# Kernel optimization log

Measured on AMD Instinct MI355X. Metric: run time of the kernel, lower is better.

## Reference

```python
import jax, jax.numpy as jnp
import numpy as np

B, T, C, H, D = 4, 2048, 1024, 16, 64
EPS = 1e-5

def setup_inputs() -> dict:
    key = jax.random.key(0)
    ks = jax.random.split(key, 8)
    s = lambda fan_in: 1.0 / np.sqrt(fan_in)
    return {
        'x': jax.random.normal(ks[0], (B, T, C), jnp.float32),
        'wq': jax.random.normal(ks[1], (H, C, D), jnp.float32) * s(C),
        'wk': jax.random.normal(ks[2], (H, C, D), jnp.float32) * s(C),
        'wv': jax.random.normal(ks[3], (H, C, D), jnp.float32) * s(C),
        'w_proj': jax.random.normal(ks[4], (C, C), jnp.float32) * s(C),
        'b_proj': jnp.zeros((C,), jnp.float32),
        'w1': jax.random.normal(ks[5], (C, 4 * C), jnp.float32) * s(C),
        'b1': jnp.zeros((4 * C,), jnp.float32),
        'w2': jax.random.normal(ks[6], (4 * C, C), jnp.float32) * s(4 * C),
        'b2': jnp.zeros((C,), jnp.float32),
        'g1': jnp.ones((C,), jnp.float32),
        'be1': jnp.zeros((C,), jnp.float32),
        'g2': jnp.ones((C,), jnp.float32),
        'be2': jnp.zeros((C,), jnp.float32),
    }

def layer_norm(x, g, b):
    mu = jnp.mean(x, axis=-1, keepdims=True)
    var = jnp.mean(jnp.square(x - mu), axis=-1, keepdims=True)
    return (x - mu) * jax.lax.rsqrt(var + EPS) * g + b

def reference(x, wq, wk, wv, w_proj, b_proj, w1, b1, w2, b2, g1, be1, g2, be2):
    # --- attention (pre-LN) ---
    xn = layer_norm(x, g1, be1)
    q = jnp.einsum('btc,hcd->bhtd', xn, wq)
    k = jnp.einsum('btc,hcd->bhtd', xn, wk)
    v = jnp.einsum('btc,hcd->bhtd', xn, wv)
    # NOTE: original scales by full embedding dim C (not head size)
    scores = jnp.einsum('bhtd,bhsd->bhts', q, k) * (C ** -0.5)
    causal = jnp.tril(jnp.ones((T, T), bool))
    scores = jnp.where(causal, scores, -jnp.inf)
    wei = jax.nn.softmax(scores, axis=-1)
    attn = jnp.einsum('bhts,bhsd->bhtd', wei, v)
    attn = attn.transpose(0, 2, 1, 3).reshape(B, T, C)  # concat heads
    x = x + attn @ w_proj + b_proj
    # --- FFN (pre-LN) ---
    xn2 = layer_norm(x, g2, be2)
    h = jax.nn.relu(xn2 @ w1 + b1)
    x = x + h @ w2 + b2
    return x
```

## Files before the change

kernel.cpp:

```cpp
#include <hip/hip_runtime.h>
#include <hip/hip_bf16.h>

#define B_ 4
#define T_ 2048
#define C_ 1024
#define H_ 16
#define D_ 64
#define M_ (B_*T_)

typedef unsigned short ushort;
typedef __attribute__((ext_vector_type(8))) short short8;
typedef __attribute__((ext_vector_type(8))) unsigned short ushort8;
typedef __attribute__((ext_vector_type(4))) float floatx4;
typedef __attribute__((ext_vector_type(4))) unsigned int uintx4;

static __device__ __forceinline__ float bf2f(ushort u) {
    unsigned int x = ((unsigned int)u) << 16;
    return __builtin_bit_cast(float, x);
}
static __device__ __forceinline__ ushort f2bf(float f) {
    unsigned int x = __builtin_bit_cast(unsigned int, f);
    unsigned int r = (x + 0x7fffu + ((x >> 16) & 1u)) >> 16;
    return (ushort)r;
}

typedef const __attribute__((address_space(1))) unsigned int gu32;
typedef __attribute__((address_space(3))) unsigned int lu32;
static __device__ __forceinline__ void glds16(const void* g, void* l) {
    __builtin_amdgcn_global_load_lds((gu32*)g, (lu32*)l, 16, 0, 0);
}

__global__ __launch_bounds__(256) void ln_kernel(
    const float* __restrict__ x, const float* __restrict__ g,
    const float* __restrict__ be, ushort* __restrict__ out)
{
    int row = blockIdx.x;
    int tid = threadIdx.x;
    const float* xr = x + (size_t)row * C_;
    float v[4];
    float s = 0.f, s2 = 0.f;
#pragma unroll
    for (int i = 0; i < 4; i++) {
        float t = xr[tid + i * 256];
        v[i] = t; s += t; s2 += t * t;
    }
#pragma unroll
    for (int off = 32; off; off >>= 1) {
        s  += __shfl_down(s, off);
        s2 += __shfl_down(s2, off);
    }
    __shared__ float rs[4], rs2[4];
    __shared__ float smu, srstd;
    int w = tid >> 6;
    if ((tid & 63) == 0) { rs[w] = s; rs2[w] = s2; }
    __syncthreads();
    if (tid == 0) {
        float ts  = rs[0] + rs[1] + rs[2] + rs[3];
        float ts2 = rs2[0] + rs2[1] + rs2[2] + rs2[3];
        float mu  = ts * (1.f / C_);
        float var = ts2 * (1.f / C_) - mu * mu;
        smu = mu; srstd = rsqrtf(var + 1e-5f);
    }
    __syncthreads();
    float mu = smu, r = srstd;
#pragma unroll
    for (int i = 0; i < 4; i++) {
        int c = tid + i * 256;
        out[(size_t)row * C_ + c] = f2bf((v[i] - mu) * r * g[c] + be[c]);
    }
}

__global__ __launch_bounds__(256) void transpose_conv(
    const float* __restrict__ in, ushort* __restrict__ out,
    int R, int Cn, long long in_bstride, long long out_bstride)
{
    __shared__ float tile[32][33];
    const float* ip = in + (size_t)blockIdx.z * in_bstride;
    ushort* op = out + (size_t)blockIdx.z * out_bstride;
    int tx = threadIdx.x;
    int ty = threadIdx.y;
    int c0 = blockIdx.x * 32, r0 = blockIdx.y * 32;
#pragma unroll
    for (int i = 0; i < 32; i += 8) {
        tile[ty + i][tx] = ip[(size_t)(r0 + ty + i) * Cn + c0 + tx];
    }
    __syncthreads();
#pragma unroll
    for (int i = 0; i < 32; i += 8) {
        int oc = c0 + ty + i;
        int orr = r0 + tx;
        op[(size_t)oc * R + orr] = f2bf(tile[tx][ty + i]);
    }
}

__global__ __launch_bounds__(256) void vtrans_kernel(
    const ushort* __restrict__ qkv, ushort* __restrict__ VtG)
{
    int bh = blockIdx.y;
    int b = bh >> 4, h = bh & 15;
    int j0 = blockIdx.x * 64;
    int tid = threadIdx.x;
    __shared__ unsigned int X[64 * 33];
    const ushort* Vg = qkv + (size_t)(b * T_) * 3072 + 2048 + h * 64;
#pragma unroll
    for (int it = 0; it < 2; it++) {
        int j = (tid >> 3) + it * 32;
        int dp = (tid & 7) * 4;
        uintx4 val = *(const uintx4*)(Vg + (size_t)(j0 + j) * 3072 + dp * 2);
#pragma unroll
        for (int k = 0; k < 4; k++) X[j * 33 + dp + k] = val[k];
    }
    __syncthreads();
    int dp = tid >> 3, jc = tid & 7;
    unsigned int v[8];
#pragma unroll
    for (int jj = 0; jj < 8; jj++) v[jj] = X[(jc * 8 + jj) * 33 + dp];
    ushort8 lo, hi;
#pragma unroll
    for (int jj = 0; jj < 8; jj++) {
        lo[jj] = (ushort)(v[jj] & 0xffffu);
        hi[jj] = (ushort)(v[jj] >> 16);
    }
    size_t r0 = ((size_t)(h * 256 + 4 * (2 * dp) + b)) * T_ + j0 + jc * 8;
    size_t r1 = ((size_t)(h * 256 + 4 * (2 * dp + 1) + b)) * T_ + j0 + jc * 8;
    *(ushort8*)&VtG[r0] = lo;
    *(ushort8*)&VtG[r1] = hi;
}

template<bool OUTBF16, bool BIAS, bool RELU, bool RESID>
__global__ __launch_bounds__(512, 2) void gemm3b_kernel(
    const ushort* __restrict__ A,
    const ushort* __restrict__ Bt,
    const float* __restrict__ bias,
    const float* __restrict__ resid,
    void* __restrict__ Cout,
    int Mdim, int Ndim, int K)
{
    __shared__ ushort As[3][256 * 64];
    __shared__ ushort Bs[3][128 * 64];

    int gridX = gridDim.x;
    int nwg = gridX * gridDim.y;
    int bid = blockIdx.y * gridX + blockIdx.x;
    int cpx = nwg >> 3;
    int swz = (bid & 7) * cpx + (bid >> 3);
    int bx = swz % gridX, by = swz / gridX;
    int m0 = by * 256, n0 = bx * 128;

    int tid = threadIdx.x;
    int wave = tid >> 6, lane = tid & 63;
    int quad = lane >> 4, l16 = lane & 15;
    int wr = wave >> 1, wc = wave & 1;
    int wm = wr * 64, wn = wc * 64;
    int lrow = lane >> 3;
    int lchunk = (lane & 7) ^ (lrow & 7);

    floatx4 acc[4][4] = {};
    int nt = K >> 6;

    auto stage = [&](int t, int sb) {
        int k0 = t << 6;
#pragma unroll
        for (int it = 0; it < 4; it++) {
            int rb = it * 64 + wave * 8;
            glds16(A + (size_t)(m0 + rb + lrow) * K + k0 + lchunk * 8, &As[sb][rb * 64]);
        }
#pragma unroll
        for (int it = 0; it < 2; it++) {
            int rb = it * 64 + wave * 8;
            glds16(Bt + (size_t)(n0 + rb + lrow) * K + k0 + lchunk * 8, &Bs[sb][rb * 64]);
        }
    };

    stage(0, 0);
    stage(1, 1);
    asm volatile("s_waitcnt vmcnt(6)" ::: "memory");
    __builtin_amdgcn_s_barrier();
    asm volatile("" ::: "memory");

    int s0 = 0, s1 = 1, s2 = 2;
    for (int t = 0; t < nt; ++t) {
        short8 af[4][2], bfv[4][2];
#pragma unroll
        for (int kk = 0; kk < 2; kk++) {
            int c = kk * 4 + quad;
#pragma unroll
            for (int mi = 0; mi < 4; mi++) {
                int r = wm + mi * 16 + l16;
                af[mi][kk] = *(const short8*)&As[s0][r * 64 + ((c ^ (r & 7)) * 8)];
            }
#pragma unroll
            for (int ni = 0; ni < 4; ni++) {
                int r = wn + ni * 16 + l16;
                bfv[ni][kk] = *(const short8*)&Bs[s0][r * 64 + ((c ^ (r & 7)) * 8)];
            }
        }
        bool pf = (t + 2 < nt);
        if (pf) stage(t + 2, s2);
        __builtin_amdgcn_s_setprio(1);
#pragma unroll
        for (int kk = 0; kk < 2; kk++)
#pragma unroll
            for (int mi = 0; mi < 4; mi++)
#pragma unroll
                for (int ni = 0; ni < 4; ni++)
                    acc[mi][ni] = __builtin_amdgcn_mfma_f32_16x16x32_bf16(
                        af[mi][kk], bfv[ni][kk], acc[mi][ni], 0, 0, 0);
        __builtin_amdgcn_s_setprio(0);
        if (pf) asm volatile("s_waitcnt vmcnt(6)" ::: "memory");
        else    asm volatile("s_waitcnt vmcnt(0)" ::: "memory");
        __builtin_amdgcn_s_barrier();
        asm volatile("" ::: "memory");
        int tmp = s0; s0 = s1; s1 = s2; s2 = tmp;
    }

    int r4 = quad * 4;
#pragma unroll
    for (int mi = 0; mi < 4; mi++) {
#pragma unroll
        for (int ni = 0; ni < 4; ni++) {
#pragma unroll
            for (int r = 0; r < 4; r++) {
                int gm = m0 + wm + mi * 16 + r4 + r;
                int gn = n0 + wn + ni * 16 + l16;
                float v = acc[mi][ni][r];
                if (BIAS)  v += bias[gn];
                if (RESID) v += resid[(size_t)gm * Ndim + gn];
                if (RELU)  v = fmaxf(v, 0.f);
                if (OUTBF16) ((ushort*)Cout)[(size_t)gm * Ndim + gn] = f2bf(v);
                else         ((float*)Cout)[(size_t)gm * Ndim + gn] = v;
            }
        }
    }
}

__global__ __launch_bounds__(256, 2) void attn_kernel(
    const ushort* __restrict__ qkv,
    const ushort* __restrict__ VtG,
    ushort* __restrict__ attnb)
{
    const int LD = 3072;
    int bid = blockIdx.x;
    int bh = (bid & 7) * 8 + ((bid >> 3) & 7);
    int qt = 15 - (bid >> 6);
    int b = bh >> 4, h = bh & 15;
    int t0 = qt * 128;
    int tid = threadIdx.x;
    int wave = tid >> 6, lane = tid & 63;
    int quad = lane >> 4, l16 = lane & 15;

    __shared__ ushort Ks[2][64 * 64];
    __shared__ ushort Vt[2][64 * 64];
    __shared__ ushort Ps[4][32 * 72];

    const ushort* Qg = qkv + (size_t)(b * T_) * LD + h * 64;
    const ushort* Kg = Qg + 1024;
    const ushort* VtB = VtG + (size_t)(h * 256 + b) * T_;

    int qrow_base = t0 + wave * 32;
    int lrow = lane >> 3;
    int lchunk = (lane & 7) ^ (lrow & 7);

    short8 qa[2][2];
#pragma unroll
    for (int mt = 0; mt < 2; mt++) {
        const ushort* qp = Qg + (size_t)(qrow_base + mt * 16 + l16) * LD + quad * 8;
        ushort8 q0 = *(const ushort8*)qp;
        ushort8 q1 = *(const ushort8*)(qp + 32);
        ushort8 a0, a1;
#pragma unroll
        for (int d = 0; d < 8; d++) {
            a0[d] = f2bf(bf2f(q0[d]) * 0.03125f);
            a1[d] = f2bf(bf2f(q1[d]) * 0.03125f);
        }
        qa[mt][0] = __builtin_bit_cast(short8, a0);
        qa[mt][1] = __builtin_bit_cast(short8, a1);
    }

    float l_part[2][4];
    floatx4 o_acc[2][4];
#pragma unroll
    for (int mt = 0; mt < 2; mt++)
#pragma unroll
        for (int r = 0; r < 4; r++) {
            l_part[mt][r] = 0.f;
            o_acc[mt][r] = floatx4{0.f, 0.f, 0.f, 0.f};
        }

    int nIter = t0 / 64 + 2;

#pragma unroll
    for (int it = 0; it < 2; it++) {
        int rb = (wave * 2 + it) * 8;
        int r = rb + lrow;
        glds16(Kg  + (size_t)r * LD + lchunk * 8, &Ks[0][rb * 64]);
        glds16(VtB + (size_t)r * (4 * T_) + lchunk * 8, &Vt[0][rb * 64]);
    }

    for (int ii = 0; ii < nIter; ii++) {
        int s0 = ii * 64;
        int buf = ii & 1;
        __syncthreads();
        if (ii + 1 < nIter) {
            int sn = s0 + 64;
#pragma unroll
            for (int it = 0; it < 2; it++) {
                int rb = (wave * 2 + it) * 8;
                int r = rb + lrow;
                glds16(Kg  + (size_t)(sn + r) * LD + lchunk * 8, &Ks[buf ^ 1][rb * 64]);
                glds16(VtB + (size_t)r * (4 * T_) + sn + lchunk * 8, &Vt[buf ^ 1][rb * 64]);
            }
        }

        if (s0 <= qrow_base + 31) {
#pragma unroll
            for (int mt = 0; mt < 2; mt++) {
                floatx4 s_acc[4];
#pragma unroll
                for (int nt = 0; nt < 4; nt++) {
                    int krow = nt * 16 + l16;
                    const short8* kb0 = (const short8*)&Ks[buf][krow * 64 + ((quad       ^ (l16 & 7)) * 8)];
                    const short8* kb1 = (const short8*)&Ks[buf][krow * 64 + (((4 + quad) ^ (l16 & 7)) * 8)];
                    floatx4 z = {0.f, 0.f, 0.f, 0.f};
                    z = __builtin_amdgcn_mfma_f32_16x16x32_bf16(qa[mt][0], *kb0, z, 0, 0, 0);
                    s_acc[nt] = __builtin_amdgcn_mfma_f32_16x16x32_bf16(qa[mt][1], *kb1, z, 0, 0, 0);
                }
                int base_mt = qrow_base + mt * 16;
                if (s0 + 63 > base_mt) {
#pragma unroll
                    for (int nt = 0; nt < 4; nt++)
#pragma unroll
                        for (int r = 0; r < 4; r++) {
                            int gi = base_mt + quad * 4 + r;
                            int gj = s0 + nt * 16 + l16;
                            if (gj > gi) s_acc[nt][r] = -INFINITY;
                        }
                }
#pragma unroll
                for (int nt = 0; nt < 4; nt++)
#pragma unroll
                    for (int r = 0; r < 4; r++) {
                        float e = __expf(s_acc[nt][r]);
                        s_acc[nt][r] = e;
                        l_part[mt][r] += e;
                        Ps[wave][(mt * 16 + quad * 4 + r) * 72 + nt * 16 + l16] = f2bf(e);
                    }
            }
            asm volatile("s_waitcnt lgkmcnt(0)" ::: "memory");
            short8 pa[2][2];
#pragma unroll
            for (int mt = 0; mt < 2; mt++) {
                pa[mt][0] = *(const short8*)&Ps[wave][(mt * 16 + l16) * 72 + quad * 8];
                pa[mt][1] = *(const short8*)&Ps[wave][(mt * 16 + l16) * 72 + quad * 8 + 32];
            }
#pragma unroll
            for (int dt = 0; dt < 4; dt++) {
                int vrow = dt * 16 + l16;
                const short8* vb0 = (const short8*)&Vt[buf][vrow * 64 + ((quad       ^ (l16 & 7)) * 8)];
                const short8* vb1 = (const short8*)&Vt[buf][vrow * 64 + (((4 + quad) ^ (l16 & 7)) * 8)];
#pragma unroll
                for (int mt = 0; mt < 2; mt++) {
                    o_acc[mt][dt] = __builtin_amdgcn_mfma_f32_16x16x32_bf16(pa[mt][0], *vb0, o_acc[mt][dt], 0, 0, 0);
                    o_acc[mt][dt] = __builtin_amdgcn_mfma_f32_16x16x32_bf16(pa[mt][1], *vb1, o_acc[mt][dt], 0, 0, 0);
                }
            }
        }
    }

#pragma unroll
    for (int mt = 0; mt < 2; mt++)
#pragma unroll
        for (int r = 0; r < 4; r++) {
            float ls = l_part[mt][r];
            ls += __shfl_xor(ls, 1);
            ls += __shfl_xor(ls, 2);
            ls += __shfl_xor(ls, 4);
            ls += __shfl_xor(ls, 8);
            float inv = 1.f / ls;
            int gi = qrow_base + mt * 16 + quad * 4 + r;
            ushort* op = attnb + (size_t)(b * T_ + gi) * 1024 + h * 64;
#pragma unroll
            for (int dt = 0; dt < 4; dt++)
                op[dt * 16 + l16] = f2bf(o_acc[mt][dt][r] * inv);
        }
}

extern "C" void kernel_launch(void* const* d_in, const int* in_sizes, int n_in,
                              void* d_out, int out_size, void* d_ws, size_t ws_size,
                              hipStream_t stream) {
    (void)in_sizes; (void)n_in; (void)out_size; (void)ws_size;
    const float* x      = (const float*)d_in[0];
    const float* wq     = (const float*)d_in[1];
    const float* wk     = (const float*)d_in[2];
    const float* wv     = (const float*)d_in[3];
    const float* w_proj = (const float*)d_in[4];
    const float* b_proj = (const float*)d_in[5];
    const float* w1     = (const float*)d_in[6];
    const float* b1     = (const float*)d_in[7];
    const float* w2     = (const float*)d_in[8];
    const float* b2     = (const float*)d_in[9];
    const float* g1     = (const float*)d_in[10];
    const float* be1    = (const float*)d_in[11];
    const float* g2     = (const float*)d_in[12];
    const float* be2    = (const float*)d_in[13];
    float* out = (float*)d_out;

    char* ws = (char*)d_ws;
    const size_t MB = 1024ull * 1024ull;
    ushort* xn     = (ushort*)(ws + 0);
    ushort* qkv    = (ushort*)(ws + 16 * MB);
    ushort* attnb  = (ushort*)(ws + 64 * MB);
    ushort* hbuf   = (ushort*)(ws + 16 * MB);
    float*  x1     = (float*) (ws + 80 * MB);
    ushort* VtG    = (ushort*)(ws + 80 * MB);
    ushort* WqkvT  = (ushort*)(ws + 112 * MB);
    ushort* WprojT = (ushort*)(ws + 118 * MB);
    ushort* W1T    = (ushort*)(ws + 120 * MB);
    ushort* W2T    = (ushort*)(ws + 128 * MB);
    ushort* xn2 = xn;

    dim3 tb(32, 8);
    ln_kernel<<<M_, 256, 0, stream>>>(x, g1, be1, xn);
    transpose_conv<<<dim3(D_ / 32, C_ / 32, H_), tb, 0, stream>>>(wq, WqkvT,               C_, D_, (long long)C_ * D_, (long long)D_ * C_);
    transpose_conv<<<dim3(D_ / 32, C_ / 32, H_), tb, 0, stream>>>(wk, WqkvT + C_ * C_,     C_, D_, (long long)C_ * D_, (long long)D_ * C_);
    transpose_conv<<<dim3(D_ / 32, C_ / 32, H_), tb, 0, stream>>>(wv, WqkvT + 2 * C_ * C_, C_, D_, (long long)C_ * D_, (long long)D_ * C_);
    transpose_conv<<<dim3(C_ / 32, C_ / 32, 1), tb, 0, stream>>>(w_proj, WprojT, C_, C_, 0, 0);
    transpose_conv<<<dim3(4 * C_ / 32, C_ / 32, 1), tb, 0, stream>>>(w1, W1T, C_, 4 * C_, 0, 0);
    transpose_conv<<<dim3(C_ / 32, 4 * C_ / 32, 1), tb, 0, stream>>>(w2, W2T, 4 * C_, C_, 0, 0);
    gemm3b_kernel<true, false, false, false><<<dim3(3072 / 128, M_ / 256), 512, 0, stream>>>(
        xn, WqkvT, nullptr, nullptr, qkv, M_, 3072, C_);
    vtrans_kernel<<<dim3(T_ / 64, B_ * H_), 256, 0, stream>>>(qkv, VtG);
    attn_kernel<<<1024, 256, 0, stream>>>(qkv, VtG, attnb);
    gemm3b_kernel<false, true, false, true><<<dim3(C_ / 128, M_ / 256), 512, 0, stream>>>(
        attnb, WprojT, b_proj, x, x1, M_, C_, C_);
    ln_kernel<<<M_, 256, 0, stream>>>(x1, g2, be2, xn2);
    gemm3b_kernel<true, true, true, false><<<dim3(4 * C_ / 128, M_ / 256), 512, 0, stream>>>(
        xn2, W1T, b1, nullptr, hbuf, M_, 4 * C_, C_);
    gemm3b_kernel<false, true, false, true><<<dim3(C_ / 128, M_ / 256), 512, 0, stream>>>(
        hbuf, W2T, b2, x1, out, M_, C_, 4 * C_);
}
```

Baseline: 446.2 us.

## Use 128x128-tile GEMM kernel with K=32 stages for FFN layers

```diff
diff --git a/kernel.cpp b/kernel.cpp
--- a/kernel.cpp
+++ b/kernel.cpp
@@ -125,6 +125,106 @@
     size_t r1 = ((size_t)(h * 256 + 4 * (2 * dp + 1) + b)) * T_ + j0 + jc * 8;
     *(ushort8*)&VtG[r0] = lo;
     *(ushort8*)&VtG[r1] = hi;
+}
+
+template<bool OUTBF16, bool BIAS, bool RELU, bool RESID>
+__global__ __launch_bounds__(256, 3) void gemm128_kernel(
+    const ushort* __restrict__ A,
+    const ushort* __restrict__ Bt,
+    const float* __restrict__ bias,
+    const float* __restrict__ resid,
+    void* __restrict__ Cout,
+    int Mdim, int Ndim, int K)
+{
+    __shared__ ushort As[3][128 * 32];
+    __shared__ ushort Bs[3][128 * 32];
+
+    int gridX = gridDim.x;
+    int nwg = gridX * gridDim.y;
+    int bid = blockIdx.y * gridX + blockIdx.x;
+    int cpx = nwg >> 3;
+    int swz = (bid & 7) * cpx + (bid >> 3);
+    int bx = swz % gridX, by = swz / gridX;
+    int m0 = by * 128, n0 = bx * 128;
+
+    int tid = threadIdx.x;
+    int wave = tid >> 6, lane = tid & 63;
+    int quad = lane >> 4, l16 = lane & 15;
+    int wm = (wave >> 1) * 64, wn = (wave & 1) * 64;
+    int lrow = lane >> 2;
+    int lchunk = (lane & 3) ^ (lrow & 3);
+
+    floatx4 acc[4][4] = {};
+    int nt = K >> 5;
+
+    auto stage = [&](int t, int sb) {
+        int k0 = t << 5;
+#pragma unroll
+        for (int it = 0; it < 2; it++) {
+            int rb = (it * 4 + wave) * 16;
+            glds16(A + (size_t)(m0 + rb + lrow) * K + k0 + lchunk * 8, &As[sb][rb * 32]);
+        }
+#pragma unroll
+        for (int it = 0; it < 2; it++) {
+            int rb = (it * 4 + wave) * 16;
+            glds16(Bt + (size_t)(n0 + rb + lrow) * K + k0 + lchunk * 8, &Bs[sb][rb * 32]);
+        }
+    };
+
+    stage(0, 0);
+    stage(1, 1);
+    asm volatile("s_waitcnt vmcnt(4)" ::: "memory");
+    __builtin_amdgcn_s_barrier();
+    asm volatile("" ::: "memory");
+
+    int s0 = 0, s1 = 1, s2 = 2;
+    for (int t = 0; t < nt; ++t) {
+        short8 af[4], bfv[4];
+#pragma unroll
+        for (int mi = 0; mi < 4; mi++) {
+            int r = wm + mi * 16 + l16;
+            af[mi] = *(const short8*)&As[s0][r * 32 + ((quad ^ (r & 3)) * 8)];
+        }
+#pragma unroll
+        for (int ni = 0; ni < 4; ni++) {
+            int r = wn + ni * 16 + l16;
+            bfv[ni] = *(const short8*)&Bs[s0][r * 32 + ((quad ^ (r & 3)) * 8)];
+        }
+        bool pf = (t + 2 < nt);
+        if (pf) stage(t + 2, s2);
+        __builtin_amdgcn_s_setprio(1);
+#pragma unroll
+        for (int mi = 0; mi < 4; mi++)
+#pragma unroll
+            for (int ni = 0; ni < 4; ni++)
+                acc[mi][ni] = __builtin_amdgcn_mfma_f32_16x16x32_bf16(
+                    af[mi], bfv[ni], acc[mi][ni], 0, 0, 0);
+        __builtin_amdgcn_s_setprio(0);
+        if (pf) asm volatile("s_waitcnt vmcnt(4)" ::: "memory");
+        else    asm volatile("s_waitcnt vmcnt(0)" ::: "memory");
+        __builtin_amdgcn_s_barrier();
+        asm volatile("" ::: "memory");
+        int tmp = s0; s0 = s1; s1 = s2; s2 = tmp;
+    }
+
+    int r4 = quad * 4;
+#pragma unroll
+    for (int mi = 0; mi < 4; mi++) {
+#pragma unroll
+        for (int ni = 0; ni < 4; ni++) {
+#pragma unroll
+            for (int r = 0; r < 4; r++) {
+                int gm = m0 + wm + mi * 16 + r4 + r;
+                int gn = n0 + wn + ni * 16 + l16;
+                float v = acc[mi][ni][r];
+                if (BIAS)  v += bias[gn];
+                if (RESID) v += resid[(size_t)gm * Ndim + gn];
+                if (RELU)  v = fmaxf(v, 0.f);
+                if (OUTBF16) ((ushort*)Cout)[(size_t)gm * Ndim + gn] = f2bf(v);
+                else         ((float*)Cout)[(size_t)gm * Ndim + gn] = v;
+            }
+        }
+    }
 }
 
 template<bool OUTBF16, bool BIAS, bool RELU, bool RESID>
@@ -434,8 +534,8 @@
     gemm3b_kernel<false, true, false, true><<<dim3(C_ / 128, M_ / 256), 512, 0, stream>>>(
         attnb, WprojT, b_proj, x, x1, M_, C_, C_);
     ln_kernel<<<M_, 256, 0, stream>>>(x1, g2, be2, xn2);
-    gemm3b_kernel<true, true, true, false><<<dim3(4 * C_ / 128, M_ / 256), 512, 0, stream>>>(
+    gemm128_kernel<true, true, true, false><<<dim3(4 * C_ / 128, M_ / 128), 256, 0, stream>>>(
         xn2, W1T, b1, nullptr, hbuf, M_, 4 * C_, C_);
-    gemm3b_kernel<false, true, false, true><<<dim3(C_ / 128, M_ / 256), 512, 0, stream>>>(
+    gemm128_kernel<false, true, false, true><<<dim3(C_ / 128, M_ / 128), 256, 0, stream>>>(
         hbuf, W2T, b2, x1, out, M_, C_, 4 * C_);
 }
```

Result: slower. 497.1 us (+11.4%).

## Add 256x256-tile ping-pong GEMM kernel for the FFN up-projection

Applied to the files above, without the earlier changes.

```diff
diff --git a/kernel.cpp b/kernel.cpp
--- a/kernel.cpp
+++ b/kernel.cpp
@@ -125,6 +125,150 @@
     size_t r1 = ((size_t)(h * 256 + 4 * (2 * dp + 1) + b)) * T_ + j0 + jc * 8;
     *(ushort8*)&VtG[r0] = lo;
     *(ushort8*)&VtG[r1] = hi;
+}
+
+template<bool OUTBF16, bool BIAS, bool RELU, bool RESID>
+__global__ __launch_bounds__(512, 2) void gemm8p_kernel(
+    const ushort* __restrict__ A,
+    const ushort* __restrict__ Bt,
+    const float* __restrict__ bias,
+    const float* __restrict__ resid,
+    void* __restrict__ Cout,
+    int Mdim, int Ndim, int K)
+{
+    __shared__ ushort AL[2][2][128 * 64];
+    __shared__ ushort BL[2][2][128 * 64];
+
+    int gridX = gridDim.x;
+    int nwg = gridX * gridDim.y;
+    int bid = blockIdx.y * gridX + blockIdx.x;
+    int cpx = nwg >> 3;
+    int swz = (bid & 7) * cpx + (bid >> 3);
+    int bx = swz % gridX, by = swz / gridX;
+    int m0 = by * 256, n0 = bx * 256;
+
+    int tid = threadIdx.x;
+    int wave = tid >> 6, lane = tid & 63;
+    int quad = lane >> 4, l16 = lane & 15;
+    int wr = wave >> 2, wc = wave & 3;
+    int lrow = lane >> 3;
+    int lchunk = (lane & 7) ^ (lrow & 7);
+
+    int nt = K >> 6;
+
+    auto stA = [&](int t, int b, int h) {
+        if (t >= nt) t = nt - 1;
+#pragma unroll
+        for (int it = 0; it < 2; it++) {
+            int rb = it * 64 + wave * 8;
+            glds16(A + (size_t)(m0 + h * 128 + rb + lrow) * K + (t << 6) + lchunk * 8,
+                   &AL[b][h][rb * 64]);
+        }
+    };
+    auto stB = [&](int t, int b, int h) {
+        if (t >= nt) t = nt - 1;
+#pragma unroll
+        for (int it = 0; it < 2; it++) {
+            int rb = it * 64 + wave * 8;
+            glds16(Bt + (size_t)(n0 + h * 128 + rb + lrow) * K + (t << 6) + lchunk * 8,
+                   &BL[b][h][rb * 64]);
+        }
+    };
+
+    floatx4 acc[8][4] = {};
+    short8 Bf[4][2];
+    short8 Af[2][2];
+
+    auto rdB = [&](int b) {
+#pragma unroll
+        for (int n = 0; n < 4; n++) {
+            int nr = wc * 64 + n * 16 + l16;
+            int h = nr >> 7, r = nr & 127;
+#pragma unroll
+            for (int kk = 0; kk < 2; kk++)
+                Bf[n][kk] = *(const short8*)&BL[b][h][r * 64 + (((kk * 4 + quad) ^ (r & 7)) * 8)];
+        }
+    };
+    auto rdA = [&](int b, int q) {
+#pragma unroll
+        for (int mi = 0; mi < 2; mi++) {
+            int R = q * 64 + wr * 32 + mi * 16 + l16;
+            int h = R >> 7, r = R & 127;
+#pragma unroll
+            for (int kk = 0; kk < 2; kk++)
+                Af[mi][kk] = *(const short8*)&AL[b][h][r * 64 + (((kk * 4 + quad) ^ (r & 7)) * 8)];
+        }
+    };
+    auto mmq = [&](int q) {
+        __builtin_amdgcn_s_setprio(1);
+#pragma unroll
+        for (int kk = 0; kk < 2; kk++)
+#pragma unroll
+            for (int mi = 0; mi < 2; mi++)
+#pragma unroll
+                for (int n = 0; n < 4; n++)
+                    acc[q * 2 + mi][n] = __builtin_amdgcn_mfma_f32_16x16x32_bf16(
+                        Af[mi][kk], Bf[n][kk], acc[q * 2 + mi][n], 0, 0, 0);
+        __builtin_amdgcn_s_setprio(0);
+    };
+
+#define BAR()   __builtin_amdgcn_s_barrier()
+#define LGKM0() asm volatile("s_waitcnt lgkmcnt(0)" ::: "memory")
+#define SCHB()  __builtin_amdgcn_sched_barrier(0)
+#define VM4()   asm volatile("s_waitcnt vmcnt(4)" ::: "memory")
+
+    stB(0, 0, 0); stB(0, 0, 1); stA(0, 0, 0); stA(0, 0, 1);
+    stB(1, 1, 0); stB(1, 1, 1);
+    VM4();
+    BAR();
+
+    int J = nt >> 1;
+    for (int j = 0; j < J; j++) {
+        int ta = 2 * j, tb = 2 * j + 1;
+        rdB(0); rdA(0, 0);  stA(tb, 1, 0);
+        BAR(); LGKM0(); SCHB(); mmq(0); BAR();
+        rdA(0, 1);          stA(tb, 1, 1); stB(ta + 2, 0, 0);
+        BAR(); LGKM0(); SCHB(); mmq(1); BAR();
+        rdA(0, 2);          stB(ta + 2, 0, 1);
+        BAR(); LGKM0(); SCHB(); mmq(2); BAR();
+        rdA(0, 3);
+        BAR(); LGKM0(); SCHB(); mmq(3);
+        VM4();
+        BAR();
+        rdB(1); rdA(1, 0);  stA(ta + 2, 0, 0);
+        BAR(); LGKM0(); SCHB(); mmq(0); BAR();
+        rdA(1, 1);          stA(ta + 2, 0, 1);
+        BAR(); LGKM0(); SCHB(); mmq(1); BAR();
+        rdA(1, 2);          stB(tb + 2, 1, 0);
+        BAR(); LGKM0(); SCHB(); mmq(2); BAR();
+        rdA(1, 3);          stB(tb + 2, 1, 1);
+        BAR(); LGKM0(); SCHB(); mmq(3);
+        VM4();
+        BAR();
+    }
+#undef BAR
+#undef LGKM0
+#undef SCHB
+#undef VM4
+
+#pragma unroll
+    for (int am = 0; am < 8; am++) {
+        int q = am >> 1, mi = am & 1;
+#pragma unroll
+        for (int n = 0; n < 4; n++) {
+#pragma unroll
+            for (int r = 0; r < 4; r++) {
+                int gm = m0 + q * 64 + wr * 32 + mi * 16 + quad * 4 + r;
+                int gn = n0 + wc * 64 + n * 16 + l16;
+                float v = acc[am][n][r];
+                if (BIAS)  v += bias[gn];
+                if (RESID) v += resid[(size_t)gm * Ndim + gn];
+                if (RELU)  v = fmaxf(v, 0.f);
+                if (OUTBF16) ((ushort*)Cout)[(size_t)gm * Ndim + gn] = f2bf(v);
+                else         ((float*)Cout)[(size_t)gm * Ndim + gn] = v;
+            }
+        }
+    }
 }
 
 template<bool OUTBF16, bool BIAS, bool RELU, bool RESID>
@@ -434,7 +578,7 @@
     gemm3b_kernel<false, true, false, true><<<dim3(C_ / 128, M_ / 256), 512, 0, stream>>>(
         attnb, WprojT, b_proj, x, x1, M_, C_, C_);
     ln_kernel<<<M_, 256, 0, stream>>>(x1, g2, be2, xn2);
-    gemm3b_kernel<true, true, true, false><<<dim3(4 * C_ / 128, M_ / 256), 512, 0, stream>>>(
+    gemm8p_kernel<true, true, true, false><<<dim3(4 * C_ / 256, M_ / 256), 512, 0, stream>>>(
         xn2, W1T, b1, nullptr, hbuf, M_, 4 * C_, C_);
     gemm3b_kernel<false, true, false, true><<<dim3(C_ / 128, M_ / 256), 512, 0, stream>>>(
         hbuf, W2T, b2, x1, out, M_, C_, 4 * C_);
```

Result: slower. 475.3 us (+6.5%).
